# Performance work log

Measured on AMD Instinct MI355X. Metric: run time of the kernel, lower is better.

The kernel has to match this reference:

```python
import jax, jax.numpy as jnp
import numpy as np

# Module config (mirrors TritonMoEConfig)
N_EMBD = 768
EXPERT_SIZES = [(8, 512), (8, 1024)]  # (count, width) pairs
TOP_K = 8
NORM_TOPK_PROB = True

EXPERT_WIDTHS = []
for cnt, w in EXPERT_SIZES:
    EXPERT_WIDTHS += [w] * cnt
EXPERT_OFFSETS = np.concatenate([[0], np.cumsum(EXPERT_WIDTHS)]).astype(np.int64)
NUM_EXPERTS = len(EXPERT_WIDTHS)          # 16
TOTAL_WIDTH = int(EXPERT_OFFSETS[-1])     # 12288


def setup_inputs() -> dict:
    key = jax.random.key(0)
    k1, k2, k3, k4 = jax.random.split(key, 4)
    x = jax.random.normal(k1, (1, 2048, N_EMBD), dtype=jnp.float32)
    # trunc_normal(std=0.02) approximated by clipped normal
    router_w = jax.random.normal(k2, (NUM_EXPERTS, N_EMBD), dtype=jnp.float32) * 0.02
    w1 = jnp.clip(jax.random.normal(k3, (N_EMBD, TOTAL_WIDTH), dtype=jnp.float32) * 0.02, -0.06, 0.06)
    w2 = jnp.clip(jax.random.normal(k4, (TOTAL_WIDTH, N_EMBD), dtype=jnp.float32) * 0.02, -0.06, 0.06)
    return {"x": x, "router_w": router_w, "w1": w1, "w2": w2}


def reference(x, router_w, w1, w2):
    B, S, D = x.shape
    xt = x.reshape(-1, D)                              # [T, D]
    T = xt.shape[0]
    # 1. Route tokens: softmax over experts, top-k selection
    logits = jnp.einsum('td,ed->te', xt, router_w)     # [T, E]
    probs = jax.nn.softmax(logits, axis=-1)
    topk_w, topk_idx = jax.lax.top_k(probs, TOP_K)     # [T, K]
    if NORM_TOPK_PROB:
        topk_w = topk_w / jnp.sum(topk_w, axis=-1, keepdims=True)
    # Per-token combine weight for every expert (0 if not selected): [T, E]
    comb = jnp.zeros((T, NUM_EXPERTS), dtype=xt.dtype)
    comb = comb.at[jnp.arange(T)[:, None], topk_idx].add(topk_w)
    # 2-6. Grouped GEMM up (with activation) + down, combine with routing weights.
    # Experts have distinct widths, so loop over the fixed expert list.
    out = jnp.zeros_like(xt)
    for e in range(NUM_EXPERTS):
        off = int(EXPERT_OFFSETS[e])
        wd = EXPERT_WIDTHS[e]
        h = jax.nn.gelu(xt @ w1[:, off:off + wd])      # [T, wd]
        out = out + comb[:, e:e + 1] * (h @ w2[off:off + wd, :])
    return out.reshape(B, S, D)
```

## Files before the change

kernel.cpp:

```cpp
#include <hip/hip_runtime.h>
#include <hip/hip_bf16.h>


#define T_TOK 2048
#define D_EMB 768
#define W_TOT 12288
#define N_EXP 16

typedef __attribute__((ext_vector_type(4))) float f32x4;
typedef __attribute__((ext_vector_type(8))) short bf16x8;

typedef __attribute__((address_space(1))) const unsigned int as1c_u32;
typedef __attribute__((address_space(3))) unsigned int as3_u32;

__device__ __forceinline__ void gload16(const void* g, void* l) {
  __builtin_amdgcn_global_load_lds((as1c_u32*)g, (as3_u32*)l, 16, 0, 0);
}

__device__ __forceinline__ unsigned short f2bf(float f) {
  __hip_bfloat16 h = __float2bfloat16(f);
  return *reinterpret_cast<unsigned short*>(&h);
}

__device__ __forceinline__ float gelu_f(float x) {
  float x3 = x * x * x;
  float a = 0.7978845608028654f * __builtin_fmaf(0.044715f, x3, x);
  a = fminf(fmaxf(a, -20.f), 20.f);
  float e = __expf(-2.0f * a);
  float t = (1.0f - e) / (1.0f + e);
  return 0.5f * x * (1.0f + t);
}


__global__ __launch_bounds__(256) void cvt_bf16_kernel(
    const float* __restrict__ in, unsigned short* __restrict__ out, int n) {
  int i = (blockIdx.x * 256 + threadIdx.x) * 4;
  if (i >= n) return;
  float4 v = *(const float4*)(in + i);
  ushort4 o;
  o.x = f2bf(v.x); o.y = f2bf(v.y); o.z = f2bf(v.z); o.w = f2bf(v.w);
  *(ushort4*)(out + i) = o;
}

__global__ __launch_bounds__(256) void transpose_cvt_kernel(
    const float* __restrict__ in, unsigned short* __restrict__ out, int R, int C) {
  __shared__ float tile[32][33];
  int c0 = blockIdx.x * 32;
  int r0 = blockIdx.y * 32;
  int i = threadIdx.x;
  {
    int r = i >> 3, c4 = (i & 7) * 4;
    float4 v = *(const float4*)(in + (size_t)(r0 + r) * C + c0 + c4);
    tile[r][c4 + 0] = v.x; tile[r][c4 + 1] = v.y;
    tile[r][c4 + 2] = v.z; tile[r][c4 + 3] = v.w;
  }
  __syncthreads();
  {
    int c = i >> 3, r4 = (i & 7) * 4;
    ushort4 o;
    o.x = f2bf(tile[r4 + 0][c]);
    o.y = f2bf(tile[r4 + 1][c]);
    o.z = f2bf(tile[r4 + 2][c]);
    o.w = f2bf(tile[r4 + 3][c]);
    *(ushort4*)(out + (size_t)(c0 + c) * R + r0 + r4) = o;
  }
}


__global__ __launch_bounds__(256) void router_kernel(
    const float* __restrict__ x, const float* __restrict__ rw,
    float* __restrict__ comb) {
  int tid = threadIdx.x, lane = tid & 63, w = tid >> 6;
  int t = blockIdx.x * 4 + w;
  const float* xr = x + (size_t)t * D_EMB;
  float xv[12];
#pragma unroll
  for (int i = 0; i < 12; ++i) xv[i] = xr[lane + 64 * i];
  float lg[16];
#pragma unroll
  for (int e = 0; e < 16; ++e) {
    const float* we = rw + (size_t)e * D_EMB;
    float p = 0.f;
#pragma unroll
    for (int i = 0; i < 12; ++i) p = __builtin_fmaf(xv[i], we[lane + 64 * i], p);
#pragma unroll
    for (int off = 32; off >= 1; off >>= 1) p += __shfl_xor(p, off, 64);
    lg[e] = p;
  }
  float mx = lg[0];
#pragma unroll
  for (int e = 1; e < 16; ++e) mx = fmaxf(mx, lg[e]);
  float ex[16];
#pragma unroll
  for (int e = 0; e < 16; ++e) ex[e] = __expf(lg[e] - mx);
  float selsum = 0.f, myval = 0.f;
#pragma unroll
  for (int e = 0; e < 16; ++e) {
    int rank = 0;
#pragma unroll
    for (int e2 = 0; e2 < 16; ++e2)
      rank += (ex[e2] > ex[e]) || (ex[e2] == ex[e] && e2 < e);
    bool sel = rank < 8;
    float v = sel ? ex[e] : 0.f;
    selsum += v;
    if (e == lane) myval = v;
  }
  if (lane < 16) comb[(size_t)t * N_EXP + lane] = myval / selsum;
}


template <int EPI, int MAP>
__global__ __launch_bounds__(512, 2) void gemm_kernel(
    const unsigned short* __restrict__ Ag, const unsigned short* __restrict__ Bg,
    int lda, int ldb, int ntiles, int kchunk, int nnt,
    const float* __restrict__ comb, unsigned short* __restrict__ hout,
    float* __restrict__ pout) {
  __shared__ __align__(16) char smem[114688];

  const int tid = threadIdx.x;
  const int lane = tid & 63;
  const int wid = tid >> 6;
  const int wr = wid >> 2;
  const int wc = wid & 3;

  int mt, nt, zt;
  {
    int bid = blockIdx.x;
    if (MAP == 0) {
      int xcd = bid & 7, r = bid >> 3;
      nt = xcd * 8 + (r >> 3); mt = r & 7; zt = 0;
    } else if (MAP == 1) {
      zt = bid & 7; int r = bid >> 3;
      nt = r & 3; mt = r >> 2;
    } else {
      nt = bid % nnt; int t2 = bid / nnt; mt = t2 & 7; zt = t2 >> 3;
    }
  }
  const int rm0 = mt * 256;
  const int cn0 = nt * 192;
  const int kbeg = zt * kchunk;

  auto stageA = [&](int buf, int j, int kt) {
    int off = j * 8192 + tid * 16;
    int row = off >> 7, inrow = off & 127;
    int scol = inrow ^ ((row & 7) << 4);
    const char* src = (const char*)Ag +
        ((size_t)(rm0 + row) * lda + (kbeg + kt * 64)) * 2 + scol;
    gload16(src, smem + buf * 32768 + j * 8192 + wid * 1024);
  };
  auto stageB = [&](int buf, int j, int kt) {
    int off = j * 8192 + tid * 16;
    int row = off >> 7, inrow = off & 127;
    int scol = inrow ^ ((row & 7) << 4);
    const char* src = (const char*)Bg +
        ((size_t)(cn0 + row) * ldb + (kbeg + kt * 64)) * 2 + scol;
    gload16(src, smem + 65536 + buf * 24576 + j * 8192 + wid * 1024);
  };
  auto rdA = [&](int buf, int m, int kk) {
    int row = wr * 128 + m * 16 + (lane & 15);
    int col = (kk * 64 + (lane >> 4) * 16) ^ ((row & 7) << 4);
    return *(const bf16x8*)(smem + buf * 32768 + row * 128 + col);
  };
  auto rdB = [&](int buf, int n, int kk) {
    int row = wc * 48 + n * 16 + (lane & 15);
    int col = (kk * 64 + (lane >> 4) * 16) ^ ((row & 7) << 4);
    return *(const bf16x8*)(smem + 65536 + buf * 24576 + row * 128 + col);
  };

  f32x4 acc[8][3];
#pragma unroll
  for (int m = 0; m < 8; ++m)
#pragma unroll
    for (int n = 0; n < 3; ++n) acc[m][n] = (f32x4){0.f, 0.f, 0.f, 0.f};

  stageB(0, 0, 0); stageB(0, 1, 0); stageB(0, 2, 0);
  stageA(0, 0, 0); stageA(0, 2, 0);
  stageA(0, 1, 0); stageA(0, 3, 0);
  __builtin_amdgcn_sched_barrier(0);

  int cur = 0;
  for (int t = 0; t < ntiles; ++t) {
    const int nxt = cur ^ 1;
    const int ktn = (t + 1 < ntiles) ? t + 1 : t;
    bf16x8 af[4][2], bf[3][2];

    asm volatile("s_waitcnt vmcnt(2)" ::: "memory");
    __builtin_amdgcn_s_barrier();
    __builtin_amdgcn_sched_barrier(0);
#pragma unroll
    for (int m = 0; m < 4; ++m)
#pragma unroll
      for (int kk = 0; kk < 2; ++kk) af[m][kk] = rdA(cur, m, kk);
#pragma unroll
    for (int n = 0; n < 3; ++n)
#pragma unroll
      for (int kk = 0; kk < 2; ++kk) bf[n][kk] = rdB(cur, n, kk);
    stageB(nxt, 0, ktn); stageB(nxt, 1, ktn); stageB(nxt, 2, ktn);
    stageA(nxt, 0, ktn); stageA(nxt, 2, ktn);
    __builtin_amdgcn_sched_barrier(0);
    __builtin_amdgcn_s_setprio(1);
#pragma unroll
    for (int m = 0; m < 4; ++m)
#pragma unroll
      for (int n = 0; n < 3; ++n)
#pragma unroll
        for (int kk = 0; kk < 2; ++kk)
          acc[m][n] = __builtin_amdgcn_mfma_f32_16x16x32_bf16(
              af[m][kk], bf[n][kk], acc[m][n], 0, 0, 0);
    __builtin_amdgcn_s_setprio(0);

    asm volatile("s_waitcnt vmcnt(5)" ::: "memory");
    __builtin_amdgcn_s_barrier();
    __builtin_amdgcn_sched_barrier(0);
#pragma unroll
    for (int m = 0; m < 4; ++m)
#pragma unroll
      for (int kk = 0; kk < 2; ++kk) af[m][kk] = rdA(cur, 4 + m, kk);
    stageA(nxt, 1, ktn); stageA(nxt, 3, ktn);
    __builtin_amdgcn_sched_barrier(0);
    __builtin_amdgcn_s_setprio(1);
#pragma unroll
    for (int m = 0; m < 4; ++m)
#pragma unroll
      for (int n = 0; n < 3; ++n)
#pragma unroll
        for (int kk = 0; kk < 2; ++kk)
          acc[4 + m][n] = __builtin_amdgcn_mfma_f32_16x16x32_bf16(
              af[m][kk], bf[n][kk], acc[4 + m][n], 0, 0, 0);
    __builtin_amdgcn_s_setprio(0);
    cur = nxt;
  }

  asm volatile("s_waitcnt vmcnt(0)" ::: "memory");
  __syncthreads();

  const int r0 = (lane >> 4) * 4;
  const int cl = lane & 15;
  if constexpr (EPI == 1) {
    float* Cwf = (float*)smem;
    {
      int row = tid >> 1, c8 = (tid & 1) * 8;
      const float* s = comb + (size_t)(rm0 + row) * N_EXP + c8;
      *(float4*)&Cwf[row * 16 + c8] = *(const float4*)s;
      *(float4*)&Cwf[row * 16 + c8 + 4] = *(const float4*)(s + 4);
    }
    __syncthreads();
#pragma unroll
    for (int n = 0; n < 3; ++n) {
      int colg = cn0 + wc * 48 + n * 16 + cl;
      int e = (colg < 4096) ? (colg >> 9) : (8 + ((colg - 4096) >> 10));
#pragma unroll
      for (int m = 0; m < 8; ++m) {
        int rl = wr * 128 + m * 16 + r0;
#pragma unroll
        for (int r = 0; r < 4; ++r) {
          float v = gelu_f(acc[m][n][r]) * Cwf[(rl + r) * 16 + e];
          hout[(size_t)(rm0 + rl + r) * W_TOT + colg] = f2bf(v);
        }
      }
    }
  } else {
    float* pz = pout + (size_t)zt * T_TOK * D_EMB;
#pragma unroll
    for (int n = 0; n < 3; ++n) {
      int colg = cn0 + wc * 48 + n * 16 + cl;
#pragma unroll
      for (int m = 0; m < 8; ++m) {
        int rl = wr * 128 + m * 16 + r0;
#pragma unroll
        for (int r = 0; r < 4; ++r)
          pz[(size_t)(rm0 + rl + r) * D_EMB + colg] = acc[m][n][r];
      }
    }
  }
}

__global__ __launch_bounds__(256) void reduce_kernel(
    const float* __restrict__ partial, float* __restrict__ out, int splits) {
  int i = (blockIdx.x * 256 + threadIdx.x) * 4;
  if (i >= T_TOK * D_EMB) return;
  float4 s = *(const float4*)(partial + i);
  for (int sp = 1; sp < splits; ++sp) {
    float4 v = *(const float4*)(partial + (size_t)sp * T_TOK * D_EMB + i);
    s.x += v.x; s.y += v.y; s.z += v.z; s.w += v.w;
  }
  *(float4*)(out + i) = s;
}


extern "C" void kernel_launch(void* const* d_in, const int* in_sizes, int n_in,
                              void* d_out, int out_size, void* d_ws, size_t ws_size,
                              hipStream_t stream) {
  const float* x = (const float*)d_in[0];
  const float* router_w = (const float*)d_in[1];
  const float* w1 = (const float*)d_in[2];
  const float* w2 = (const float*)d_in[3];
  float* out = (float*)d_out;

  char* ws = (char*)d_ws;
  size_t off = 0;
  auto alloc = [&](size_t bytes) {
    char* p = ws + off;
    off += (bytes + 255) & ~(size_t)255;
    return p;
  };
  unsigned short* xb  = (unsigned short*)alloc((size_t)T_TOK * D_EMB * 2);
  unsigned short* w1t = (unsigned short*)alloc((size_t)W_TOT * D_EMB * 2);
  unsigned short* w2t = (unsigned short*)alloc((size_t)D_EMB * W_TOT * 2);
  unsigned short* h   = (unsigned short*)alloc((size_t)T_TOK * W_TOT * 2);
  float* comb         = (float*)alloc((size_t)T_TOK * N_EXP * 4);

  int splits = 8;
  if (off + (size_t)8 * T_TOK * D_EMB * 4 > ws_size) splits = 4;
  if (off + (size_t)4 * T_TOK * D_EMB * 4 > ws_size) splits = 2;
  float* partial = (float*)alloc((size_t)splits * T_TOK * D_EMB * 4);
  int kchunk = W_TOT / splits;

  cvt_bf16_kernel<<<(T_TOK * D_EMB) / 1024, 256, 0, stream>>>(x, xb, T_TOK * D_EMB);
  transpose_cvt_kernel<<<dim3(W_TOT / 32, D_EMB / 32), 256, 0, stream>>>(w1, w1t, D_EMB, W_TOT);
  transpose_cvt_kernel<<<dim3(D_EMB / 32, W_TOT / 32), 256, 0, stream>>>(w2, w2t, W_TOT, D_EMB);
  router_kernel<<<T_TOK / 4, 256, 0, stream>>>(x, router_w, comb);

  gemm_kernel<1, 0><<<512, 512, 0, stream>>>(
      xb, w1t, D_EMB, D_EMB, D_EMB / 64, D_EMB, 64, comb, h, nullptr);

  if (splits == 8) {
    gemm_kernel<0, 1><<<256, 512, 0, stream>>>(
        h, w2t, W_TOT, W_TOT, kchunk / 64, kchunk, 4, nullptr, nullptr, partial);
  } else {
    gemm_kernel<0, 2><<<32 * splits, 512, 0, stream>>>(
        h, w2t, W_TOT, W_TOT, kchunk / 64, kchunk, 4, nullptr, nullptr, partial);
  }
  reduce_kernel<<<(T_TOK * D_EMB) / 1024, 256, 0, stream>>>(partial, out, splits);
}
```

Baseline: 142.7 us.

## Switch GEMMs to 32x32x16 MFMA with 256x256 tiles and 4-stage K pipeline

```diff
diff --git a/kernel.cpp b/kernel.cpp
--- a/kernel.cpp
+++ b/kernel.cpp
@@ -7,7 +7,7 @@
 #define W_TOT 12288
 #define N_EXP 16
 
-typedef __attribute__((ext_vector_type(4))) float f32x4;
+typedef __attribute__((ext_vector_type(16))) float f32x16;
 typedef __attribute__((ext_vector_type(8))) short bf16x8;
 
 typedef __attribute__((address_space(1))) const unsigned int as1c_u32;
@@ -29,17 +29,6 @@
   float e = __expf(-2.0f * a);
   float t = (1.0f - e) / (1.0f + e);
   return 0.5f * x * (1.0f + t);
-}
-
-
-__global__ __launch_bounds__(256) void cvt_bf16_kernel(
-    const float* __restrict__ in, unsigned short* __restrict__ out, int n) {
-  int i = (blockIdx.x * 256 + threadIdx.x) * 4;
-  if (i >= n) return;
-  float4 v = *(const float4*)(in + i);
-  ushort4 o;
-  o.x = f2bf(v.x); o.y = f2bf(v.y); o.z = f2bf(v.z); o.w = f2bf(v.w);
-  *(ushort4*)(out + i) = o;
 }
 
 __global__ __launch_bounds__(256) void transpose_cvt_kernel(
@@ -69,13 +58,16 @@
 
 __global__ __launch_bounds__(256) void router_kernel(
     const float* __restrict__ x, const float* __restrict__ rw,
-    float* __restrict__ comb) {
+    float* __restrict__ comb, unsigned short* __restrict__ xbout) {
   int tid = threadIdx.x, lane = tid & 63, w = tid >> 6;
   int t = blockIdx.x * 4 + w;
   const float* xr = x + (size_t)t * D_EMB;
   float xv[12];
 #pragma unroll
   for (int i = 0; i < 12; ++i) xv[i] = xr[lane + 64 * i];
+#pragma unroll
+  for (int i = 0; i < 12; ++i)
+    xbout[(size_t)t * D_EMB + lane + 64 * i] = f2bf(xv[i]);
   float lg[16];
 #pragma unroll
   for (int e = 0; e < 16; ++e) {
@@ -112,10 +104,10 @@
 template <int EPI, int MAP>
 __global__ __launch_bounds__(512, 2) void gemm_kernel(
     const unsigned short* __restrict__ Ag, const unsigned short* __restrict__ Bg,
-    int lda, int ldb, int ntiles, int kchunk, int nnt,
+    int lda, int ldb, int ntiles, int kchunk,
     const float* __restrict__ comb, unsigned short* __restrict__ hout,
     float* __restrict__ pout) {
-  __shared__ __align__(16) char smem[114688];
+  __shared__ __align__(16) char smem[131072];
 
   const int tid = threadIdx.x;
   const int lane = tid & 63;
@@ -128,114 +120,95 @@
     int bid = blockIdx.x;
     if (MAP == 0) {
       int xcd = bid & 7, r = bid >> 3;
-      nt = xcd * 8 + (r >> 3); mt = r & 7; zt = 0;
-    } else if (MAP == 1) {
+      nt = xcd * 6 + (r >> 3); mt = r & 7; zt = 0;
+    } else {
       zt = bid & 7; int r = bid >> 3;
-      nt = r & 3; mt = r >> 2;
-    } else {
-      nt = bid % nnt; int t2 = bid / nnt; mt = t2 & 7; zt = t2 >> 3;
+      nt = r % 3; mt = r / 3;
     }
   }
   const int rm0 = mt * 256;
-  const int cn0 = nt * 192;
+  const int cn0 = nt * 256;
   const int kbeg = zt * kchunk;
 
-  auto stageA = [&](int buf, int j, int kt) {
+  auto stageA = [&](int b, int j, int kt) {
     int off = j * 8192 + tid * 16;
-    int row = off >> 7, inrow = off & 127;
-    int scol = inrow ^ ((row & 7) << 4);
+    int row = off >> 6;
+    int scol = (((off >> 4) & 3) ^ ((row >> 1) & 3)) << 4;
     const char* src = (const char*)Ag +
-        ((size_t)(rm0 + row) * lda + (kbeg + kt * 64)) * 2 + scol;
-    gload16(src, smem + buf * 32768 + j * 8192 + wid * 1024);
-  };
-  auto stageB = [&](int buf, int j, int kt) {
+        ((size_t)(rm0 + row) * lda + (kbeg + kt * 32)) * 2 + scol;
+    gload16(src, smem + b * 16384 + j * 8192 + wid * 1024);
+  };
+  auto stageB = [&](int b, int j, int kt) {
     int off = j * 8192 + tid * 16;
-    int row = off >> 7, inrow = off & 127;
-    int scol = inrow ^ ((row & 7) << 4);
+    int row = off >> 6;
+    int scol = (((off >> 4) & 3) ^ ((row >> 1) & 3)) << 4;
     const char* src = (const char*)Bg +
-        ((size_t)(cn0 + row) * ldb + (kbeg + kt * 64)) * 2 + scol;
-    gload16(src, smem + 65536 + buf * 24576 + j * 8192 + wid * 1024);
-  };
-  auto rdA = [&](int buf, int m, int kk) {
-    int row = wr * 128 + m * 16 + (lane & 15);
-    int col = (kk * 64 + (lane >> 4) * 16) ^ ((row & 7) << 4);
-    return *(const bf16x8*)(smem + buf * 32768 + row * 128 + col);
-  };
-  auto rdB = [&](int buf, int n, int kk) {
-    int row = wc * 48 + n * 16 + (lane & 15);
-    int col = (kk * 64 + (lane >> 4) * 16) ^ ((row & 7) << 4);
-    return *(const bf16x8*)(smem + 65536 + buf * 24576 + row * 128 + col);
-  };
-
-  f32x4 acc[8][3];
-#pragma unroll
-  for (int m = 0; m < 8; ++m)
-#pragma unroll
-    for (int n = 0; n < 3; ++n) acc[m][n] = (f32x4){0.f, 0.f, 0.f, 0.f};
-
-  stageB(0, 0, 0); stageB(0, 1, 0); stageB(0, 2, 0);
-  stageA(0, 0, 0); stageA(0, 2, 0);
-  stageA(0, 1, 0); stageA(0, 3, 0);
+        ((size_t)(cn0 + row) * ldb + (kbeg + kt * 32)) * 2 + scol;
+    gload16(src, smem + 65536 + b * 16384 + j * 8192 + wid * 1024);
+  };
+  auto rdA = [&](int b, int m, int ks) {
+    int row = wr * 128 + m * 32 + (lane & 31);
+    int col = (ks * 32 + ((lane >> 5) << 4)) ^ (((row >> 1) & 3) << 4);
+    return *(const bf16x8*)(smem + b * 16384 + row * 64 + col);
+  };
+  auto rdB = [&](int b, int n, int ks) {
+    int row = wc * 64 + n * 32 + (lane & 31);
+    int col = (ks * 32 + ((lane >> 5) << 4)) ^ (((row >> 1) & 3) << 4);
+    return *(const bf16x8*)(smem + 65536 + b * 16384 + row * 64 + col);
+  };
+
+  f32x16 acc[4][2];
+#pragma unroll
+  for (int m = 0; m < 4; ++m)
+#pragma unroll
+    for (int n = 0; n < 2; ++n)
+#pragma unroll
+      for (int r = 0; r < 16; ++r) acc[m][n][r] = 0.f;
+
+  stageA(0, 0, 0); stageA(0, 1, 0); stageB(0, 0, 0); stageB(0, 1, 0);
+  stageA(1, 0, 1); stageA(1, 1, 1); stageB(1, 0, 1); stageB(1, 1, 1);
   __builtin_amdgcn_sched_barrier(0);
 
-  int cur = 0;
+#pragma unroll 4
   for (int t = 0; t < ntiles; ++t) {
-    const int nxt = cur ^ 1;
-    const int ktn = (t + 1 < ntiles) ? t + 1 : t;
-    bf16x8 af[4][2], bf[3][2];
-
-    asm volatile("s_waitcnt vmcnt(2)" ::: "memory");
+    const int b = t & 3;
+    const int nb = (t + 2) & 3;
+    const int kt2 = (t + 2 < ntiles) ? t + 2 : ntiles - 1;
+
+    asm volatile("s_waitcnt vmcnt(4)" ::: "memory");
     __builtin_amdgcn_s_barrier();
     __builtin_amdgcn_sched_barrier(0);
+
+    bf16x8 af[4][2], bf[2][2];
 #pragma unroll
     for (int m = 0; m < 4; ++m)
 #pragma unroll
-      for (int kk = 0; kk < 2; ++kk) af[m][kk] = rdA(cur, m, kk);
-#pragma unroll
-    for (int n = 0; n < 3; ++n)
-#pragma unroll
-      for (int kk = 0; kk < 2; ++kk) bf[n][kk] = rdB(cur, n, kk);
-    stageB(nxt, 0, ktn); stageB(nxt, 1, ktn); stageB(nxt, 2, ktn);
-    stageA(nxt, 0, ktn); stageA(nxt, 2, ktn);
+      for (int ks = 0; ks < 2; ++ks) af[m][ks] = rdA(b, m, ks);
+#pragma unroll
+    for (int n = 0; n < 2; ++n)
+#pragma unroll
+      for (int ks = 0; ks < 2; ++ks) bf[n][ks] = rdB(b, n, ks);
+
+    stageA(nb, 0, kt2); stageA(nb, 1, kt2);
+    stageB(nb, 0, kt2); stageB(nb, 1, kt2);
     __builtin_amdgcn_sched_barrier(0);
+
     __builtin_amdgcn_s_setprio(1);
 #pragma unroll
     for (int m = 0; m < 4; ++m)
 #pragma unroll
-      for (int n = 0; n < 3; ++n)
-#pragma unroll
-        for (int kk = 0; kk < 2; ++kk)
-          acc[m][n] = __builtin_amdgcn_mfma_f32_16x16x32_bf16(
-              af[m][kk], bf[n][kk], acc[m][n], 0, 0, 0);
+      for (int n = 0; n < 2; ++n)
+#pragma unroll
+        for (int ks = 0; ks < 2; ++ks)
+          acc[m][n] = __builtin_amdgcn_mfma_f32_32x32x16_bf16(
+              af[m][ks], bf[n][ks], acc[m][n], 0, 0, 0);
     __builtin_amdgcn_s_setprio(0);
-
-    asm volatile("s_waitcnt vmcnt(5)" ::: "memory");
-    __builtin_amdgcn_s_barrier();
-    __builtin_amdgcn_sched_barrier(0);
-#pragma unroll
-    for (int m = 0; m < 4; ++m)
-#pragma unroll
-      for (int kk = 0; kk < 2; ++kk) af[m][kk] = rdA(cur, 4 + m, kk);
-    stageA(nxt, 1, ktn); stageA(nxt, 3, ktn);
-    __builtin_amdgcn_sched_barrier(0);
-    __builtin_amdgcn_s_setprio(1);
-#pragma unroll
-    for (int m = 0; m < 4; ++m)
-#pragma unroll
-      for (int n = 0; n < 3; ++n)
-#pragma unroll
-        for (int kk = 0; kk < 2; ++kk)
-          acc[4 + m][n] = __builtin_amdgcn_mfma_f32_16x16x32_bf16(
-              af[m][kk], bf[n][kk], acc[4 + m][n], 0, 0, 0);
-    __builtin_amdgcn_s_setprio(0);
-    cur = nxt;
   }
 
   asm volatile("s_waitcnt vmcnt(0)" ::: "memory");
   __syncthreads();
 
-  const int r0 = (lane >> 4) * 4;
-  const int cl = lane & 15;
+  const int rbase = wr * 128 + 4 * (lane >> 5);
   if constexpr (EPI == 1) {
     float* Cwf = (float*)smem;
     {
@@ -246,30 +219,32 @@
     }
     __syncthreads();
 #pragma unroll
-    for (int n = 0; n < 3; ++n) {
-      int colg = cn0 + wc * 48 + n * 16 + cl;
-      int e = (colg < 4096) ? (colg >> 9) : (8 + ((colg - 4096) >> 10));
-#pragma unroll
-      for (int m = 0; m < 8; ++m) {
-        int rl = wr * 128 + m * 16 + r0;
-#pragma unroll
-        for (int r = 0; r < 4; ++r) {
-          float v = gelu_f(acc[m][n][r]) * Cwf[(rl + r) * 16 + e];
-          hout[(size_t)(rm0 + rl + r) * W_TOT + colg] = f2bf(v);
+    for (int n = 0; n < 2; ++n) {
+      int colg0 = cn0 + wc * 64 + n * 32;
+      int e = (colg0 < 4096) ? (colg0 >> 9) : (8 + ((colg0 - 4096) >> 10));
+      int col = colg0 + (lane & 31);
+#pragma unroll
+      for (int m = 0; m < 4; ++m) {
+#pragma unroll
+        for (int r = 0; r < 16; ++r) {
+          int rl = rbase + m * 32 + (r & 3) + 8 * (r >> 2);
+          float v = gelu_f(acc[m][n][r]) * Cwf[rl * 16 + e];
+          hout[(size_t)(rm0 + rl) * W_TOT + col] = f2bf(v);
         }
       }
     }
   } else {
     float* pz = pout + (size_t)zt * T_TOK * D_EMB;
 #pragma unroll
-    for (int n = 0; n < 3; ++n) {
-      int colg = cn0 + wc * 48 + n * 16 + cl;
-#pragma unroll
-      for (int m = 0; m < 8; ++m) {
-        int rl = wr * 128 + m * 16 + r0;
-#pragma unroll
-        for (int r = 0; r < 4; ++r)
-          pz[(size_t)(rm0 + rl + r) * D_EMB + colg] = acc[m][n][r];
+    for (int n = 0; n < 2; ++n) {
+      int col = cn0 + wc * 64 + n * 32 + (lane & 31);
+#pragma unroll
+      for (int m = 0; m < 4; ++m) {
+#pragma unroll
+        for (int r = 0; r < 16; ++r) {
+          int rl = rbase + m * 32 + (r & 3) + 8 * (r >> 2);
+          pz[(size_t)(rm0 + rl) * D_EMB + col] = acc[m][n][r];
+        }
       }
     }
   }
@@ -310,26 +285,19 @@
   unsigned short* h   = (unsigned short*)alloc((size_t)T_TOK * W_TOT * 2);
   float* comb         = (float*)alloc((size_t)T_TOK * N_EXP * 4);
 
-  int splits = 8;
-  if (off + (size_t)8 * T_TOK * D_EMB * 4 > ws_size) splits = 4;
-  if (off + (size_t)4 * T_TOK * D_EMB * 4 > ws_size) splits = 2;
+  const int splits = 8;
   float* partial = (float*)alloc((size_t)splits * T_TOK * D_EMB * 4);
   int kchunk = W_TOT / splits;
 
-  cvt_bf16_kernel<<<(T_TOK * D_EMB) / 1024, 256, 0, stream>>>(x, xb, T_TOK * D_EMB);
   transpose_cvt_kernel<<<dim3(W_TOT / 32, D_EMB / 32), 256, 0, stream>>>(w1, w1t, D_EMB, W_TOT);
   transpose_cvt_kernel<<<dim3(D_EMB / 32, W_TOT / 32), 256, 0, stream>>>(w2, w2t, W_TOT, D_EMB);
-  router_kernel<<<T_TOK / 4, 256, 0, stream>>>(x, router_w, comb);
-
-  gemm_kernel<1, 0><<<512, 512, 0, stream>>>(
-      xb, w1t, D_EMB, D_EMB, D_EMB / 64, D_EMB, 64, comb, h, nullptr);
-
-  if (splits == 8) {
-    gemm_kernel<0, 1><<<256, 512, 0, stream>>>(
-        h, w2t, W_TOT, W_TOT, kchunk / 64, kchunk, 4, nullptr, nullptr, partial);
-  } else {
-    gemm_kernel<0, 2><<<32 * splits, 512, 0, stream>>>(
-        h, w2t, W_TOT, W_TOT, kchunk / 64, kchunk, 4, nullptr, nullptr, partial);
-  }
+  router_kernel<<<T_TOK / 4, 256, 0, stream>>>(x, router_w, comb, xb);
+
+  gemm_kernel<1, 0><<<384, 512, 0, stream>>>(
+      xb, w1t, D_EMB, D_EMB, D_EMB / 32, D_EMB, comb, h, nullptr);
+
+  gemm_kernel<0, 1><<<192, 512, 0, stream>>>(
+      h, w2t, W_TOT, W_TOT, kchunk / 32, kchunk, nullptr, nullptr, partial);
+
   reduce_kernel<<<(T_TOK * D_EMB) / 1024, 256, 0, stream>>>(partial, out, splits);
 }
```

After: 173.0 us. +21.2%, slower.
